# Kernel optimization log

Measured on AMD Instinct MI355X. Metric: run time of the kernel, lower is better.

Reference implementation:

```python
import jax, jax.numpy as jnp
import numpy as np

B, C_IN, H, W = 8, 1024, 18, 80
FEAT = 1024
A = 32      # anchors per location
NCLS = 3    # classes
NREG = 13
K = 3       # kernel size
K2 = K * K
EPS = 1e-5  # BatchNorm eps


def conv2d(x, w, b):
    y = jax.lax.conv_general_dilated(x, w, (1, 1), ((1, 1), (1, 1)),
                                     dimension_numbers=('NCHW', 'OIHW', 'NCHW'))
    return y + b[None, :, None, None]


def bn_eval(x, g, b):
    # eval-mode BatchNorm2d with running_mean=0, running_var=1
    return x * (g / jnp.sqrt(1.0 + EPS))[None, :, None, None] + b[None, :, None, None]


def anchor_flatten(x, d):
    # [B, A*d, H, W] -> permute(0,2,3,1) -> [B, H*W*A, d]
    Bx, Cx, Hx, Wx = x.shape
    return jnp.transpose(x, (0, 2, 3, 1)).reshape(Bx, Hx * Wx * (Cx // d), d)


def bilinear_gather(x, py, px):
    # x: [B,C,H,W]; py/px: [B,K2,H,W] float coords -> [B,C,K2,H,W], zero outside
    Bx, Cx, Hx, Wx = x.shape
    y0 = jnp.floor(py); x0 = jnp.floor(px)
    wy1 = py - y0; wx1 = px - x0
    wy0 = 1.0 - wy1; wx0 = 1.0 - wx1
    xf = x.reshape(Bx, Cx, Hx * Wx)

    def g(yy, xx):
        valid = ((yy >= 0) & (yy < Hx) & (xx >= 0) & (xx < Wx)).astype(x.dtype)
        yc = jnp.clip(yy, 0, Hx - 1).astype(jnp.int32)
        xc = jnp.clip(xx, 0, Wx - 1).astype(jnp.int32)
        idx = (yc * Wx + xc).reshape(Bx, -1)
        vals = jax.vmap(lambda xi, ii: xi[:, ii])(xf, idx).reshape(Bx, Cx, K2, Hx, Wx)
        return vals * valid[:, None]

    return (g(y0, x0) * (wy0 * wx0)[:, None] + g(y0, x0 + 1) * (wy0 * wx1)[:, None]
            + g(y0 + 1, x0) * (wy1 * wx0)[:, None] + g(y0 + 1, x0 + 1) * (wy1 * wx1)[:, None])


def mdcn(x, off_w, off_b, w, b):
    # ModulatedDeformConvPack (DCNv2): 3x3 conv -> (dy, dx, mask), then modulated deform conv
    out = conv2d(x, off_w, off_b)                        # [B, 3*K2, H, W]
    dy, dx, m = out[:, :K2], out[:, K2:2 * K2], jax.nn.sigmoid(out[:, 2 * K2:])
    ky, kx = jnp.meshgrid(jnp.arange(K, dtype=x.dtype), jnp.arange(K, dtype=x.dtype), indexing='ij')
    base_y = jnp.arange(x.shape[2], dtype=x.dtype)[None, None, :, None] - 1.0 + ky.reshape(1, K2, 1, 1)
    base_x = jnp.arange(x.shape[3], dtype=x.dtype)[None, None, None, :] - 1.0 + kx.reshape(1, K2, 1, 1)
    sampled = bilinear_gather(x, base_y + dy, base_x + dx) * m[:, None]   # [B,C,K2,H,W]
    O = w.shape[0]
    return jnp.einsum('bckhw,ock->bohw', sampled, w.reshape(O, w.shape[1], K2)) + b[None, :, None, None]


def setup_inputs() -> dict:
    key = jax.random.key(0)
    ks = jax.random.split(key, 10)
    s1 = 1.0 / np.sqrt(C_IN * K2)
    s2 = 1.0 / np.sqrt(FEAT * K2)
    rn = lambda k, sh, sc: jax.random.normal(k, sh, jnp.float32) * sc
    return {
        'features': jax.random.normal(ks[0], (B, C_IN, H, W), jnp.float32),
        'cls_w1': rn(ks[1], (FEAT, C_IN, K, K), s1), 'cls_b1': jnp.zeros((FEAT,), jnp.float32),
        'cls_w2': rn(ks[2], (FEAT, FEAT, K, K), s2), 'cls_b2': jnp.zeros((FEAT,), jnp.float32),
        'cls_w3': rn(ks[3], (A * NCLS, FEAT, K, K), s2), 'cls_b3': jnp.zeros((A * NCLS,), jnp.float32),
        'off_w': rn(ks[4], (3 * K2, C_IN, K, K), s1), 'off_b': jnp.zeros((3 * K2,), jnp.float32),
        'dcn_w': rn(ks[5], (FEAT, C_IN, K, K), s1), 'dcn_b': jnp.zeros((FEAT,), jnp.float32),
        'bn1_g': jnp.ones((FEAT,), jnp.float32), 'bn1_b': jnp.zeros((FEAT,), jnp.float32),
        'reg_w2': rn(ks[6], (FEAT, FEAT, K, K), s2), 'reg_b2': jnp.zeros((FEAT,), jnp.float32),
        'bn2_g': jnp.ones((FEAT,), jnp.float32), 'bn2_b': jnp.zeros((FEAT,), jnp.float32),
        'reg_w3': rn(ks[7], (A * NREG, FEAT, K, K), s2), 'reg_b3': jnp.zeros((A * NREG,), jnp.float32),
    }


def reference(features, cls_w1, cls_b1, cls_w2, cls_b2, cls_w3, cls_b3,
              off_w, off_b, dcn_w, dcn_b, bn1_g, bn1_b,
              reg_w2, reg_b2, bn2_g, bn2_b, reg_w3, reg_b3):
    # cls branch (Dropout2d is identity in eval)
    h = jax.nn.relu(conv2d(features, cls_w1, cls_b1))
    h = jax.nn.relu(conv2d(h, cls_w2, cls_b2))
    cls_preds = anchor_flatten(conv2d(h, cls_w3, cls_b3), NCLS)   # [B, H*W*A, NCLS]
    # reg branch: modulated deformable conv -> BN -> ReLU -> conv -> BN -> ReLU -> conv
    r = jax.nn.relu(bn_eval(mdcn(features, off_w, off_b, dcn_w, dcn_b), bn1_g, bn1_b))
    r = jax.nn.relu(bn_eval(conv2d(r, reg_w2, reg_b2), bn2_g, bn2_b))
    reg_preds = anchor_flatten(conv2d(r, reg_w3, reg_b3), NREG)   # [B, H*W*A, NREG]
    return (cls_preds, reg_preds)
```

## Files before the change

### kernel.cpp

```cpp
#include <hip/hip_runtime.h>
#include <math.h>

typedef short short8 __attribute__((ext_vector_type(8)));
typedef float f32x4 __attribute__((ext_vector_type(4)));
typedef unsigned short u16;
typedef unsigned int u32;

#define GAS(p) ((__attribute__((address_space(1))) void*)(p))
#define LAS(p) ((__attribute__((address_space(3))) void*)(p))

namespace {

constexpr int HW   = 1440;
constexpr int PBAT = 20 * 82 * 1024;

__device__ __forceinline__ u16 f2bf(float f) {
  u32 u = __float_as_uint(f);
  return (u16)((u + 0x7FFFu + ((u >> 16) & 1u)) >> 16);
}
__device__ __forceinline__ float bf2f(u16 h) {
  return __uint_as_float(((u32)h) << 16);
}

__global__ __launch_bounds__(256)
void transpose_feat(const float* __restrict__ src, u16* __restrict__ dst) {
  __shared__ float tile[128][17];
  const int bh = blockIdx.y;
  const int b = bh / 18, h = bh % 18;
  const int wt = blockIdx.x % 5, ct = blockIdx.x / 5;
  const int w0 = wt * 16, c0 = ct * 128;
  const int tid = threadIdx.x;
#pragma unroll
  for (int it = 0; it < 8; ++it) {
    int idx = it * 256 + tid;
    int c = idx >> 4, w = idx & 15;
    tile[c][w] = src[((size_t)(b * 1024 + c0 + c) * 18 + h) * 80 + w0 + w];
  }
  __syncthreads();
  const int px = tid >> 4, cq = tid & 15;
  union { uint4 u; u16 s[8]; } pk;
#pragma unroll
  for (int j = 0; j < 8; ++j) pk.s[j] = f2bf(tile[cq * 8 + j][px]);
  *(uint4*)(dst + ((size_t)(b * 20 + h + 1) * 82 + (w0 + px + 1)) * 1024 + c0 + cq * 8) = pk.u;
}

struct RepackArgs {
  const float* src[7];
  u16* dst[7];
  int O[7];
  int start[7];
  int nseg;
};

__global__ __launch_bounds__(256)
void repack_all(RepackArgs ra) {
  int blk = blockIdx.x;
  int seg = 0;
#pragma unroll
  for (int i = 1; i < 7; ++i)
    if (i < ra.nseg && blk >= ra.start[i]) seg = i;
  const float* src = ra.src[seg];
  u16* dst = ra.dst[seg];
  const int O = ra.O[seg];
  int idx = (blk - ra.start[seg]) * 256 + threadIdx.x;
  if (idx >= O * 128) return;
  int o = idx >> 7, c8 = idx & 127;
  const float* s = src + (size_t)o * 9216 + (size_t)c8 * 72;
  float v[72];
#pragma unroll
  for (int i = 0; i < 18; ++i) {
    float4 f = *(const float4*)(s + i * 4);
    v[i * 4 + 0] = f.x; v[i * 4 + 1] = f.y; v[i * 4 + 2] = f.z; v[i * 4 + 3] = f.w;
  }
#pragma unroll
  for (int t = 0; t < 9; ++t) {
    union { uint4 u; u16 h[8]; } pk;
#pragma unroll
    for (int j = 0; j < 8; ++j) pk.h[j] = f2bf(v[j * 9 + t]);
    *(uint4*)(dst + ((size_t)t * O + o) * 1024 + c8 * 8) = pk.u;
  }
}

__device__ __forceinline__
void sample_body(int k, int lp, int pix0, int Npc,
                 const u16* __restrict__ featP, const float* __restrict__ offp,
                 u16* __restrict__ spl, int tid) {
  const int p = pix0 + lp;
  const int c8 = tid & 15;
  int b = p / HW, hw = p - b * HW;
  int h = hw / 80, w = hw - h * 80;
  float dy = offp[p * 27 + k];
  float dx = offp[p * 27 + 9 + k];
  float ml = offp[p * 27 + 18 + k];
  float m = 1.f / (1.f + expf(-ml));
  float py = (float)(h - 1 + k / 3) + dy;
  float px = (float)(w - 1 + (k % 3)) + dx;
  float y0f = floorf(py), x0f = floorf(px);
  float wy1 = py - y0f, wx1 = px - x0f;
  float wy0 = 1.f - wy1, wx0 = 1.f - wx1;
  int y0 = (int)y0f, x0 = (int)x0f;
  int ya = min(max(y0, -1), 18),  yb = min(max(y0 + 1, -1), 18);
  int xa = min(max(x0, -1), 80),  xb = min(max(x0 + 1, -1), 80);
  const u16* base = featP + (size_t)b * PBAT;
  const u16* r00 = base + ((size_t)(ya + 1) * 82 + (xa + 1)) * 1024;
  const u16* r01 = base + ((size_t)(ya + 1) * 82 + (xb + 1)) * 1024;
  const u16* r10 = base + ((size_t)(yb + 1) * 82 + (xa + 1)) * 1024;
  const u16* r11 = base + ((size_t)(yb + 1) * 82 + (xb + 1)) * 1024;
  float w00 = wy0 * wx0 * m, w01 = wy0 * wx1 * m;
  float w10 = wy1 * wx0 * m, w11 = wy1 * wx1 * m;
  u16* dst = spl + ((size_t)k * Npc + lp) * 1024;
  for (int c = c8 * 8; c < 1024; c += 128) {
    union { uint4 u; u16 h[8]; } a, bq, cq2, d, o;
    a.u   = *(const uint4*)(r00 + c);
    bq.u  = *(const uint4*)(r01 + c);
    cq2.u = *(const uint4*)(r10 + c);
    d.u   = *(const uint4*)(r11 + c);
#pragma unroll
    for (int j = 0; j < 8; ++j) {
      float v = w00 * bf2f(a.h[j]) + w01 * bf2f(bq.h[j]) +
                w10 * bf2f(cq2.h[j]) + w11 * bf2f(d.h[j]);
      o.h[j] = f2bf(v);
    }
    *(uint4*)(dst + c) = o.u;
  }
}

__global__ __launch_bounds__(256)
void sample_standalone(const u16* __restrict__ featP, const float* __restrict__ offp,
                       u16* __restrict__ spl, int pix0, int Npc) {
  sample_body(blockIdx.y, blockIdx.x * 16 + (threadIdx.x >> 4), pix0, Npc,
              featP, offp, spl, threadIdx.x);
}

struct Job {
  const u16* W; const u16* B;
  const float* bias; const float* bng; const float* bnb;
  void* out; int Co; int pix0; int Npc;
};

template<int FLAGS>
__device__ __forceinline__ void gemm_body(const Job J, int px, int oy) {
  constexpr bool PLANES  = (FLAGS & 1) != 0;
  constexpr bool F32OUT  = (FLAGS & 2) != 0;
  constexpr bool HASBN   = (FLAGS & 4) != 0;
  constexpr bool HASRELU = (FLAGS & 8) != 0;

  __shared__ __align__(16) u16 As[128 * 32];
  __shared__ __align__(16) u16 Bs[128 * 32];
  const int tid = threadIdx.x;
  const int wv = tid >> 6, lane = tid & 63;
  const int o0 = oy * 128;
  const int p0 = J.pix0 + px * 128;

  const int lr = lane >> 2;
  const int qs = (lane & 3) ^ ((lane >> 3) & 3);
  int aoff[2], boff[2];
#pragma unroll
  for (int s = 0; s < 2; ++s) {
    int r = (wv * 2 + s) * 16 + lr;
    int o = min(o0 + r, J.Co - 1);
    aoff[s] = o * 1024 + qs * 8;
    int p = p0 + r;
    if (PLANES) {
      boff[s] = (p - J.pix0) * 1024 + qs * 8;
    } else {
      int b = p / HW, hw = p - b * HW;
      int h = hw / 80, w = hw - h * 80;
      boff[s] = ((b * 20 + h) * 82 + w) * 1024 + qs * 8;
    }
  }
  u16* aDst = As + (wv * 2) * 512;
  u16* bDst = Bs + (wv * 2) * 512;

  const int wm = wv >> 1, wn = wv & 1;
  const int frm = lane & 15;
  const int kq = lane >> 4;
  const int sel = (kq ^ ((lane >> 1) & 3)) * 16;

  f32x4 acc[4][4];
#pragma unroll
  for (int i = 0; i < 4; ++i)
#pragma unroll
    for (int j = 0; j < 4; ++j) acc[i][j] = (f32x4)0.f;

  for (int t = 0; t < 9; ++t) {
    const u16* Wt = J.W + (size_t)t * J.Co * 1024;
    const u16* Bt = J.B + (PLANES ? (size_t)t * (size_t)J.Npc * 1024
                                  : (size_t)(((t / 3) * 82 + (t % 3)) * 1024));
    for (int cc = 0; cc < 1024; cc += 32) {
      __syncthreads();
#pragma unroll
      for (int s = 0; s < 2; ++s) {
        __builtin_amdgcn_global_load_lds(GAS(Wt + aoff[s] + cc), LAS(aDst + s * 512), 16, 0, 0);
        __builtin_amdgcn_global_load_lds(GAS(Bt + boff[s] + cc), LAS(bDst + s * 512), 16, 0, 0);
      }
      __syncthreads();
      uint4 af[4], bf4[4];
#pragma unroll
      for (int i = 0; i < 4; ++i) {
        af[i]  = *(const uint4*)((const char*)As + (wm * 64 + i * 16 + frm) * 64 + sel);
        bf4[i] = *(const uint4*)((const char*)Bs + (wn * 64 + i * 16 + frm) * 64 + sel);
      }
#pragma unroll
      for (int i = 0; i < 4; ++i) {
        short8 a = __builtin_bit_cast(short8, af[i]);
#pragma unroll
        for (int j = 0; j < 4; ++j) {
          short8 b = __builtin_bit_cast(short8, bf4[j]);
          acc[i][j] = __builtin_amdgcn_mfma_f32_16x16x32_bf16(a, b, acc[i][j], 0, 0, 0);
        }
      }
    }
  }

  size_t obase[4];
#pragma unroll
  for (int j = 0; j < 4; ++j) {
    int pn = p0 + wn * 64 + j * 16 + frm;
    if (F32OUT) {
      obase[j] = (size_t)pn * J.Co;
    } else {
      int b = pn / HW, hw = pn - b * HW;
      int h = hw / 80, w = hw - h * 80;
      obase[j] = ((size_t)(b * 20 + h + 1) * 82 + (w + 1)) * 1024;
    }
  }
#pragma unroll
  for (int i = 0; i < 4; ++i) {
    int o = o0 + wm * 64 + i * 16 + kq * 4;
    float bi[4], sc[4], sh[4];
#pragma unroll
    for (int r = 0; r < 4; ++r) {
      int oc = min(o + r, J.Co - 1);
      bi[r] = J.bias[oc];
      if (HASBN) { sc[r] = J.bng[oc] * rsqrtf(1.f + 1e-5f); sh[r] = J.bnb[oc]; }
    }
#pragma unroll
    for (int j = 0; j < 4; ++j) {
      float v[4];
#pragma unroll
      for (int r = 0; r < 4; ++r) {
        float x = acc[i][j][r] + bi[r];
        if (HASBN) x = x * sc[r] + sh[r];
        if (HASRELU) x = fmaxf(x, 0.f);
        v[r] = x;
      }
      if (F32OUT) {
        float* op = (float*)J.out;
#pragma unroll
        for (int r = 0; r < 4; ++r)
          if (o + r < J.Co) op[obase[j] + o + r] = v[r];
      } else {
        u16* op = (u16*)J.out;
        ushort4 pk;
        pk.x = f2bf(v[0]); pk.y = f2bf(v[1]); pk.z = f2bf(v[2]); pk.w = f2bf(v[3]);
        *(ushort4*)(op + obase[j] + o) = pk;
      }
    }
  }
}

template<int F0, int F1>
__global__ __launch_bounds__(256)
void gemm_dual(Job j0, Job j1, int ysplit) {
  int y = blockIdx.y;
  if (y < ysplit) gemm_body<F0>(j0, blockIdx.x, y);
  else            gemm_body<F1>(j1, blockIdx.x, y - ysplit);
}

template<int F0>
__global__ __launch_bounds__(256)
void gemm_sample(Job j, const u16* __restrict__ featP, const float* __restrict__ offp,
                 u16* __restrict__ spl, int gemmBlocks) {
  int gx = blockIdx.x;
  if (gx < gemmBlocks) {
    gemm_body<F0>(j, gx % 90, gx / 90);
  } else {
    int sidx = gx - gemmBlocks;
    int k = sidx / 720, bs = sidx % 720;
    sample_body(k, bs * 16 + (threadIdx.x >> 4), 0, 11520, featP, offp, spl, threadIdx.x);
  }
}

}

extern "C" void kernel_launch(void* const* d_in, const int* in_sizes, int n_in,
                              void* d_out, int out_size, void* d_ws, size_t ws_size,
                              hipStream_t stream) {
  const float* feat   = (const float*)d_in[0];
  const float* cls_w1 = (const float*)d_in[1];
  const float* cls_b1 = (const float*)d_in[2];
  const float* cls_w2 = (const float*)d_in[3];
  const float* cls_b2 = (const float*)d_in[4];
  const float* cls_w3 = (const float*)d_in[5];
  const float* cls_b3 = (const float*)d_in[6];
  const float* off_w  = (const float*)d_in[7];
  const float* off_b  = (const float*)d_in[8];
  const float* dcn_w  = (const float*)d_in[9];
  const float* dcn_b  = (const float*)d_in[10];
  const float* bn1_g  = (const float*)d_in[11];
  const float* bn1_b  = (const float*)d_in[12];
  const float* reg_w2 = (const float*)d_in[13];
  const float* reg_b2 = (const float*)d_in[14];
  const float* bn2_g  = (const float*)d_in[15];
  const float* bn2_b  = (const float*)d_in[16];
  const float* reg_w3 = (const float*)d_in[17];
  const float* reg_b3 = (const float*)d_in[18];
  float* outp = (float*)d_out;

  const size_t ACTB = 26869760;
  char* wsb = (char*)d_ws;
  u16* featP = (u16*)(wsb);
  u16* bufA  = (u16*)(wsb + ACTB);
  u16* bufB  = (u16*)(wsb + 2 * ACTB);
  u16* wts   = (u16*)(wsb + 3 * ACTB);
  float* offp = (float*)(wsb + 3 * ACTB + 85432320);
  u16* spl   = (u16*)(wsb + 3 * ACTB + 85432320 + 1244160);
  const size_t BASE = 3 * ACTB + 85432320 + 1244160;
  const size_t SPLB = (size_t)9 * 11520 * 1024 * 2;

  u16* offT = wts;
  u16* w1T  = wts + 248832;
  u16* w2T  = wts + 9686016;
  u16* w3T  = wts + 19123200;
  u16* dcnT = wts + 20007936;
  u16* r2T  = wts + 29445120;
  u16* r3T  = wts + 38882304;

  dim3 blk(256);

  hipMemsetAsync(featP, 0, 3 * ACTB, stream);
  transpose_feat<<<dim3(40, 144), blk, 0, stream>>>(feat, featP);

  {
    RepackArgs ra;
    const float* s[7] = {off_w, cls_w1, cls_w2, cls_w3, dcn_w, reg_w2, reg_w3};
    u16* d[7] = {offT, w1T, w2T, w3T, dcnT, r2T, r3T};
    int  O[7] = {27, 1024, 1024, 96, 1024, 1024, 416};
    int acc = 0;
    for (int i = 0; i < 7; ++i) {
      ra.src[i] = s[i]; ra.dst[i] = d[i]; ra.O[i] = O[i]; ra.start[i] = acc;
      acc += (O[i] * 128 + 255) / 256;
    }
    ra.nseg = 7;
    repack_all<<<dim3(acc), blk, 0, stream>>>(ra);
  }

  Job jOff  = {offT, featP, off_b, nullptr, nullptr, offp, 27, 0, 0};
  Job jCls1 = {w1T, featP, cls_b1, nullptr, nullptr, bufA, 1024, 0, 0};
  Job jCls2 = {w2T, bufA, cls_b2, nullptr, nullptr, bufB, 1024, 0, 0};
  Job jCls3 = {w3T, bufB, cls_b3, nullptr, nullptr, outp, 96, 0, 0};
  Job jReg2 = {r2T, bufA, reg_b2, bn2_g, bn2_b, bufB, 1024, 0, 0};
  Job jReg3 = {r3T, bufB, reg_b3, nullptr, nullptr, outp + 1105920, 416, 0, 0};

  gemm_dual<8, 2><<<dim3(90, 9), blk, 0, stream>>>(jCls1, jOff, 8);

  if (ws_size >= BASE + SPLB) {
    gemm_sample<8><<<dim3(720 + 6480), blk, 0, stream>>>(jCls2, featP, offp, spl, 720);
    Job jDcn = {dcnT, spl, dcn_b, bn1_g, bn1_b, bufA, 1024, 0, 11520};
    gemm_dual<1 | 4 | 8, 2><<<dim3(90, 9), blk, 0, stream>>>(jDcn, jCls3, 8);
  } else {
    gemm_dual<8, 8><<<dim3(90, 8), blk, 0, stream>>>(jCls2, jCls2, 8);
    size_t avail = ws_size > BASE ? ws_size - BASE : 0;
    int tiles = (int)(avail / 2359296);
    if (tiles < 1) tiles = 1;
    if (tiles > 90) tiles = 90;
    for (int t0 = 0; t0 < 90; t0 += tiles) {
      int nt = (90 - t0) < tiles ? (90 - t0) : tiles;
      int pix0 = t0 * 128, np = nt * 128;
      sample_standalone<<<dim3(nt * 8, 9), blk, 0, stream>>>(featP, offp, spl, pix0, np);
      Job jDcn = {dcnT, spl, dcn_b, bn1_g, bn1_b, bufA, 1024, pix0, np};
      gemm_dual<1 | 4 | 8, 1 | 4 | 8><<<dim3(nt, 8), blk, 0, stream>>>(jDcn, jDcn, 8);
    }
    gemm_dual<2, 2><<<dim3(90, 1), blk, 0, stream>>>(jCls3, jCls3, 1);
  }

  gemm_dual<4 | 8, 4 | 8><<<dim3(90, 8), blk, 0, stream>>>(jReg2, jReg2, 8);
  gemm_dual<2, 2><<<dim3(90, 4), blk, 0, stream>>>(jReg3, jReg3, 4);
}
```

Measured before the change: 2.157 ms.

## Add 256x256-tile 8-wave GEMM with LDS double buffering for large convs

Adds a new GEMM kernel that uses 512 threads and 256x256 output tiles. It double-buffers through a 128KB LDS with direct global-to-LDS loads and interleaves MFMA phases with staging under raised wave priority. The kernel replaces the 128-tile GEMMs for the cls1/offset, cls2+sampling, DCN and reg2 stages, and the co-scheduled sampling blocks are resized to 512 threads. The aim is more data reuse per loaded tile and better overlap of memory and math. The cost is fewer blocks (180–225), which may underfill the GPU's CUs, plus heavier LDS and register use.

```diff
diff --git a/kernel.cpp b/kernel.cpp
--- a/kernel.cpp
+++ b/kernel.cpp
@@ -268,17 +268,200 @@
   else            gemm_body<F1>(j1, blockIdx.x, y - ysplit);
 }
 
+template<int FLAGS>
+__device__ __forceinline__ void gemm8_body(const Job J, char* ldsb, int px, int oy) {
+  constexpr bool PLANES  = (FLAGS & 1) != 0;
+  constexpr bool F32OUT  = (FLAGS & 2) != 0;
+  constexpr bool HASBN   = (FLAGS & 4) != 0;
+  constexpr bool HASRELU = (FLAGS & 8) != 0;
+
+  const int tid = threadIdx.x;
+  const int w = tid >> 6, lane = tid & 63;
+  const int o0 = oy * 256;
+  const int p0 = J.pix0 + px * 256;
+
+  const int lr3 = lane >> 3;
+  const int srcC = ((lane & 7) ^ lr3) << 3;
+  u32 aEl[2][2], bEl[2][2];
+#pragma unroll
+  for (int h = 0; h < 2; ++h)
+#pragma unroll
+  for (int s = 0; s < 2; ++s) {
+    int crow = (w * 2 + s) * 8 + lr3;
+    int o = min(o0 + h * 128 + crow, J.Co - 1);
+    aEl[h][s] = (u32)o * 1024u;
+    int p = p0 + h * 128 + crow;
+    if (PLANES) {
+      bEl[h][s] = (u32)(p - J.pix0) * 1024u;
+    } else {
+      int b = p / HW, hw = p - b * HW;
+      int hh = hw / 80, ww = hw - hh * 80;
+      bEl[h][s] = (u32)((b * 20 + hh) * 82 + ww) * 1024u;
+    }
+  }
+
+  auto STAGE_A = [&](int buf, int h, int kt) {
+    int tap = kt >> 4, cc = (kt & 15) << 6;
+    const u16* src = J.W + (size_t)tap * (size_t)J.Co * 1024 + cc + srcC;
+    char* dst = ldsb + (buf * 65536 + h * 16384 + (w * 2) * 1024);
+    __builtin_amdgcn_global_load_lds(GAS(src + aEl[h][0]), LAS(dst), 16, 0, 0);
+    __builtin_amdgcn_global_load_lds(GAS(src + aEl[h][1]), LAS(dst + 1024), 16, 0, 0);
+  };
+  auto STAGE_B = [&](int buf, int h, int kt) {
+    int tap = kt >> 4, cc = (kt & 15) << 6;
+    size_t tb = PLANES ? (size_t)tap * (size_t)J.Npc * 1024
+                       : (size_t)(((tap / 3) * 82 + (tap % 3)) * 1024);
+    const u16* src = J.B + tb + cc + srcC;
+    char* dst = ldsb + (buf * 65536 + 32768 + h * 16384 + (w * 2) * 1024);
+    __builtin_amdgcn_global_load_lds(GAS(src + bEl[h][0]), LAS(dst), 16, 0, 0);
+    __builtin_amdgcn_global_load_lds(GAS(src + bEl[h][1]), LAS(dst + 1024), 16, 0, 0);
+  };
+
+  const int wm2 = w >> 2, wn2 = w & 3;
+  const int rA = wm2 * 64 + (lane & 15);
+  const int rB = wn2 * 32 + (lane & 15);
+  const int xsw = (lane & 7) << 4;
+  const int csw0 = (((lane >> 4) << 4)) ^ xsw;
+  const int csw1 = (64 | ((lane >> 4) << 4)) ^ xsw;
+
+  f32x4 acc[4][4][2];
+#pragma unroll
+  for (int q = 0; q < 4; ++q)
+#pragma unroll
+  for (int m = 0; m < 4; ++m)
+#pragma unroll
+  for (int n = 0; n < 2; ++n) acc[q][m][n] = (f32x4)0.f;
+
+  uint4 aF[4][2], bF[2][2];
+
+#define G8_RD_A(BUF, AH)                                                      \
+  { const char* Ab_ = ldsb + ((BUF) * 65536 + (AH) * 16384);                  \
+    _Pragma("unroll") for (int m_ = 0; m_ < 4; ++m_) {                        \
+      aF[m_][0] = *(const uint4*)(Ab_ + (rA + m_ * 16) * 128 + csw0);         \
+      aF[m_][1] = *(const uint4*)(Ab_ + (rA + m_ * 16) * 128 + csw1); } }
+
+#define G8_RD_B(BUF, BH)                                                      \
+  { const char* Bb_ = ldsb + ((BUF) * 65536 + 32768 + (BH) * 16384);          \
+    _Pragma("unroll") for (int n_ = 0; n_ < 2; ++n_) {                        \
+      bF[n_][0] = *(const uint4*)(Bb_ + (rB + n_ * 16) * 128 + csw0);         \
+      bF[n_][1] = *(const uint4*)(Bb_ + (rB + n_ * 16) * 128 + csw1); } }
+
+#define G8_MMA(Q)                                                             \
+    __builtin_amdgcn_s_barrier();                                             \
+    asm volatile("s_waitcnt lgkmcnt(0)" ::: "memory");                        \
+    __builtin_amdgcn_sched_barrier(0);                                        \
+    __builtin_amdgcn_s_setprio(1);                                            \
+    _Pragma("unroll") for (int m_ = 0; m_ < 4; ++m_)                          \
+    _Pragma("unroll") for (int n_ = 0; n_ < 2; ++n_)                          \
+    _Pragma("unroll") for (int k_ = 0; k_ < 2; ++k_)                          \
+      acc[Q][m_][n_] = __builtin_amdgcn_mfma_f32_16x16x32_bf16(               \
+          __builtin_bit_cast(short8, aF[m_][k_]),                             \
+          __builtin_bit_cast(short8, bF[n_][k_]), acc[Q][m_][n_], 0, 0, 0);   \
+    __builtin_amdgcn_s_setprio(0);
+
+#define G8_VMW asm volatile("s_waitcnt vmcnt(4)" ::: "memory");
+#define G8_BAR __builtin_amdgcn_s_barrier();
+
+  STAGE_A(0, 0, 0); STAGE_A(0, 1, 0); STAGE_B(0, 0, 0); STAGE_B(0, 1, 0);
+  STAGE_A(1, 0, 1); STAGE_B(1, 0, 1);
+  G8_VMW
+  __builtin_amdgcn_s_barrier();
+
+  for (int it = 0; it < 72; ++it) {
+    const int kt = it * 2;
+    const int k2 = min(kt + 2, 143), k3 = min(kt + 3, 143);
+    G8_RD_A(0, 0) G8_RD_B(0, 0) STAGE_B(1, 1, kt + 1); G8_MMA(0) G8_BAR
+    G8_RD_B(0, 1)               STAGE_A(1, 1, kt + 1); G8_MMA(1) G8_BAR
+    G8_RD_A(0, 1) G8_RD_B(0, 0) STAGE_A(0, 0, k2);     G8_MMA(2) G8_BAR
+    G8_RD_B(0, 1)               STAGE_B(0, 0, k2);     G8_MMA(3) G8_VMW G8_BAR
+    G8_RD_A(1, 0) G8_RD_B(1, 0) STAGE_B(0, 1, k2);     G8_MMA(0) G8_BAR
+    G8_RD_B(1, 1)               STAGE_A(0, 1, k2);     G8_MMA(1) G8_BAR
+    G8_RD_A(1, 1) G8_RD_B(1, 0) STAGE_A(1, 0, k3);     G8_MMA(2) G8_BAR
+    G8_RD_B(1, 1)               STAGE_B(1, 0, k3);     G8_MMA(3) G8_VMW G8_BAR
+  }
+
+#undef G8_RD_A
+#undef G8_RD_B
+#undef G8_MMA
+#undef G8_VMW
+#undef G8_BAR
+
+  const int kq = lane >> 4, fr = lane & 15;
+  size_t pixB[2][2];
+#pragma unroll
+  for (int bh = 0; bh < 2; ++bh)
+#pragma unroll
+  for (int n = 0; n < 2; ++n) {
+    int p = p0 + bh * 128 + wn2 * 32 + n * 16 + fr;
+    if (F32OUT) {
+      pixB[bh][n] = (size_t)p * J.Co;
+    } else {
+      int b = p / HW, hw = p - b * HW;
+      int hh = hw / 80, ww = hw - hh * 80;
+      pixB[bh][n] = ((size_t)(b * 20 + hh + 1) * 82 + (ww + 1)) * 1024;
+    }
+  }
+#pragma unroll
+  for (int ah = 0; ah < 2; ++ah)
+#pragma unroll
+  for (int m = 0; m < 4; ++m) {
+    int ob = o0 + ah * 128 + wm2 * 64 + m * 16 + kq * 4;
+    float bi[4], sc[4], sh[4];
+#pragma unroll
+    for (int r = 0; r < 4; ++r) {
+      int oc = min(ob + r, J.Co - 1);
+      bi[r] = J.bias[oc];
+      if (HASBN) { sc[r] = J.bng[oc] * rsqrtf(1.f + 1e-5f); sh[r] = J.bnb[oc]; }
+    }
+#pragma unroll
+    for (int bh = 0; bh < 2; ++bh)
+#pragma unroll
+    for (int n = 0; n < 2; ++n) {
+      float v[4];
+#pragma unroll
+      for (int r = 0; r < 4; ++r) {
+        float x = acc[ah * 2 + bh][m][n][r] + bi[r];
+        if (HASBN) x = x * sc[r] + sh[r];
+        if (HASRELU) x = fmaxf(x, 0.f);
+        v[r] = x;
+      }
+      if (F32OUT) {
+        float* op = (float*)J.out;
+#pragma unroll
+        for (int r = 0; r < 4; ++r)
+          if (ob + r < J.Co) op[pixB[bh][n] + ob + r] = v[r];
+      } else {
+        u16* op = (u16*)J.out;
+        ushort4 pk;
+        pk.x = f2bf(v[0]); pk.y = f2bf(v[1]); pk.z = f2bf(v[2]); pk.w = f2bf(v[3]);
+        *(ushort4*)(op + pixB[bh][n] + ob) = pk;
+      }
+    }
+  }
+}
+
+template<int F0, int F1>
+__global__ __launch_bounds__(512, 2)
+void gemm8_dual(Job j0, Job j1, int n0, int mt0, int mt1) {
+  __shared__ __align__(16) char ldsb[131072];
+  int x = blockIdx.x;
+  if (x < n0) gemm8_body<F0>(j0, ldsb, x / mt0, x % mt0);
+  else { x -= n0; gemm8_body<F1>(j1, ldsb, x / mt1, x % mt1); }
+}
+
 template<int F0>
-__global__ __launch_bounds__(256)
-void gemm_sample(Job j, const u16* __restrict__ featP, const float* __restrict__ offp,
-                 u16* __restrict__ spl, int gemmBlocks) {
-  int gx = blockIdx.x;
-  if (gx < gemmBlocks) {
-    gemm_body<F0>(j, gx % 90, gx / 90);
+__global__ __launch_bounds__(512, 2)
+void gemm8_sample(Job j, const u16* __restrict__ featP, const float* __restrict__ offp,
+                  u16* __restrict__ spl, int n0, int mt0) {
+  __shared__ __align__(16) char ldsb[131072];
+  int x = blockIdx.x;
+  if (x < n0) {
+    gemm8_body<F0>(j, ldsb, x / mt0, x % mt0);
   } else {
-    int sidx = gx - gemmBlocks;
-    int k = sidx / 720, bs = sidx % 720;
-    sample_body(k, bs * 16 + (threadIdx.x >> 4), 0, 11520, featP, offp, spl, threadIdx.x);
+    int sidx = x - n0;
+    int k = sidx / 360, bs = sidx % 360;
+    sample_body(k, bs * 32 + ((int)threadIdx.x >> 4), 0, 11520,
+                featP, offp, spl, (int)threadIdx.x);
   }
 }
 
@@ -353,13 +536,16 @@
   Job jReg2 = {r2T, bufA, reg_b2, bn2_g, bn2_b, bufB, 1024, 0, 0};
   Job jReg3 = {r3T, bufB, reg_b3, nullptr, nullptr, outp + 1105920, 416, 0, 0};
 
-  gemm_dual<8, 2><<<dim3(90, 9), blk, 0, stream>>>(jCls1, jOff, 8);
-
   if (ws_size >= BASE + SPLB) {
-    gemm_sample<8><<<dim3(720 + 6480), blk, 0, stream>>>(jCls2, featP, offp, spl, 720);
+    dim3 b512(512);
+    gemm8_dual<8, 2><<<dim3(225), b512, 0, stream>>>(jCls1, jOff, 180, 4, 1);
+    gemm8_sample<8><<<dim3(180 + 3240), b512, 0, stream>>>(jCls2, featP, offp, spl, 180, 4);
     Job jDcn = {dcnT, spl, dcn_b, bn1_g, bn1_b, bufA, 1024, 0, 11520};
-    gemm_dual<1 | 4 | 8, 2><<<dim3(90, 9), blk, 0, stream>>>(jDcn, jCls3, 8);
+    gemm8_dual<1 | 4 | 8, 2><<<dim3(225), b512, 0, stream>>>(jDcn, jCls3, 180, 4, 1);
+    gemm8_dual<4 | 8, 4 | 8><<<dim3(180), b512, 0, stream>>>(jReg2, jReg2, 180, 4, 4);
+    gemm_dual<2, 2><<<dim3(90, 4), blk, 0, stream>>>(jReg3, jReg3, 4);
   } else {
+    gemm_dual<8, 2><<<dim3(90, 9), blk, 0, stream>>>(jCls1, jOff, 8);
     gemm_dual<8, 8><<<dim3(90, 8), blk, 0, stream>>>(jCls2, jCls2, 8);
     size_t avail = ws_size > BASE ? ws_size - BASE : 0;
     int tiles = (int)(avail / 2359296);
@@ -373,8 +559,7 @@
       gemm_dual<1 | 4 | 8, 1 | 4 | 8><<<dim3(nt, 8), blk, 0, stream>>>(jDcn, jDcn, 8);
     }
     gemm_dual<2, 2><<<dim3(90, 1), blk, 0, stream>>>(jCls3, jCls3, 1);
-  }
-
-  gemm_dual<4 | 8, 4 | 8><<<dim3(90, 8), blk, 0, stream>>>(jReg2, jReg2, 8);
-  gemm_dual<2, 2><<<dim3(90, 4), blk, 0, stream>>>(jReg3, jReg3, 4);
-}
+    gemm_dual<4 | 8, 4 | 8><<<dim3(90, 8), blk, 0, stream>>>(jReg2, jReg2, 8);
+    gemm_dual<2, 2><<<dim3(90, 4), blk, 0, stream>>>(jReg3, jReg3, 4);
+  }
+}
```

Result: no change. 2.161 ms (+0.2%).

## Triple-buffer GEMM LDS staging and pipeline chunked DCN sampling with GEMM

Applied to the files above, without the earlier changes.

The GEMM inner loop moves from a single LDS buffer with two barriers per K-step to a three-stage ring. Global-to-LDS loads for step k+2 are issued before the MFMAs for step k, with vmcnt waits, so load latency is hidden. A new mid-workspace path splits the deformable sampling into chunks and double-buffers them: each launch runs the DCN GEMM on the current chunk and samples the next chunk concurrently. Triple buffering raises LDS per block to 48KB, which may reduce occupancy.

```diff
diff --git a/kernel.cpp b/kernel.cpp
--- a/kernel.cpp
+++ b/kernel.cpp
@@ -145,8 +145,8 @@
   constexpr bool HASBN   = (FLAGS & 4) != 0;
   constexpr bool HASRELU = (FLAGS & 8) != 0;
 
-  __shared__ __align__(16) u16 As[128 * 32];
-  __shared__ __align__(16) u16 Bs[128 * 32];
+  __shared__ __align__(16) u16 As[3 * 4096];
+  __shared__ __align__(16) u16 Bs[3 * 4096];
   const int tid = threadIdx.x;
   const int wv = tid >> 6, lane = tid & 63;
   const int o0 = oy * 128;
@@ -169,8 +169,6 @@
       boff[s] = ((b * 20 + h) * 82 + w) * 1024 + qs * 8;
     }
   }
-  u16* aDst = As + (wv * 2) * 512;
-  u16* bDst = Bs + (wv * 2) * 512;
 
   const int wm = wv >> 1, wn = wv & 1;
   const int frm = lane & 15;
@@ -183,35 +181,57 @@
 #pragma unroll
     for (int j = 0; j < 4; ++j) acc[i][j] = (f32x4)0.f;
 
-  for (int t = 0; t < 9; ++t) {
-    const u16* Wt = J.W + (size_t)t * J.Co * 1024;
-    const u16* Bt = J.B + (PLANES ? (size_t)t * (size_t)J.Npc * 1024
-                                  : (size_t)(((t / 3) * 82 + (t % 3)) * 1024));
-    for (int cc = 0; cc < 1024; cc += 32) {
-      __syncthreads();
-#pragma unroll
-      for (int s = 0; s < 2; ++s) {
-        __builtin_amdgcn_global_load_lds(GAS(Wt + aoff[s] + cc), LAS(aDst + s * 512), 16, 0, 0);
-        __builtin_amdgcn_global_load_lds(GAS(Bt + boff[s] + cc), LAS(bDst + s * 512), 16, 0, 0);
-      }
-      __syncthreads();
-      uint4 af[4], bf4[4];
-#pragma unroll
-      for (int i = 0; i < 4; ++i) {
-        af[i]  = *(const uint4*)((const char*)As + (wm * 64 + i * 16 + frm) * 64 + sel);
-        bf4[i] = *(const uint4*)((const char*)Bs + (wn * 64 + i * 16 + frm) * 64 + sel);
-      }
-#pragma unroll
-      for (int i = 0; i < 4; ++i) {
-        short8 a = __builtin_bit_cast(short8, af[i]);
-#pragma unroll
-        for (int j = 0; j < 4; ++j) {
-          short8 b = __builtin_bit_cast(short8, bf4[j]);
-          acc[i][j] = __builtin_amdgcn_mfma_f32_16x16x32_bf16(a, b, acc[i][j], 0, 0, 0);
-        }
-      }
-    }
-  }
+#define GB_STAGE(ST, KK)                                                      \
+  { int t_ = (KK) >> 5, c0_ = ((KK) & 31) << 5;                               \
+    const u16* Wt_ = J.W + (size_t)t_ * (size_t)J.Co * 1024 + c0_;            \
+    const u16* Bt_ = J.B + (PLANES ? (size_t)t_ * (size_t)J.Npc * 1024        \
+                     : (size_t)(((t_ / 3) * 82 + (t_ % 3)) * 1024)) + c0_;    \
+    u16* aD_ = As + (ST) * 4096 + (wv * 2) * 512;                             \
+    u16* bD_ = Bs + (ST) * 4096 + (wv * 2) * 512;                             \
+    __builtin_amdgcn_global_load_lds(GAS(Wt_ + aoff[0]), LAS(aD_),       16, 0, 0); \
+    __builtin_amdgcn_global_load_lds(GAS(Wt_ + aoff[1]), LAS(aD_ + 512), 16, 0, 0); \
+    __builtin_amdgcn_global_load_lds(GAS(Bt_ + boff[0]), LAS(bD_),       16, 0, 0); \
+    __builtin_amdgcn_global_load_lds(GAS(Bt_ + boff[1]), LAS(bD_ + 512), 16, 0, 0); }
+
+#define GB_MMA(ST)                                                            \
+  { const char* Ab_ = (const char*)As + (ST) * 8192;                          \
+    const char* Bb_ = (const char*)Bs + (ST) * 8192;                          \
+    uint4 af[4], bf4[4];                                                      \
+    _Pragma("unroll") for (int i_ = 0; i_ < 4; ++i_) {                        \
+      af[i_]  = *(const uint4*)(Ab_ + (wm * 64 + i_ * 16 + frm) * 64 + sel);  \
+      bf4[i_] = *(const uint4*)(Bb_ + (wn * 64 + i_ * 16 + frm) * 64 + sel); }\
+    _Pragma("unroll") for (int i_ = 0; i_ < 4; ++i_) {                        \
+      short8 a_ = __builtin_bit_cast(short8, af[i_]);                         \
+      _Pragma("unroll") for (int j_ = 0; j_ < 4; ++j_) {                      \
+        short8 b_ = __builtin_bit_cast(short8, bf4[j_]);                      \
+        acc[i_][j_] = __builtin_amdgcn_mfma_f32_16x16x32_bf16(a_, b_, acc[i_][j_], 0, 0, 0); } } }
+
+#define GB_STEP(ST, NB, KS, DOST, VMN)                                        \
+  { if (DOST) GB_STAGE(NB, KS)                                                \
+    GB_MMA(ST)                                                                \
+    asm volatile("s_waitcnt vmcnt(" #VMN ")" ::: "memory");                   \
+    __builtin_amdgcn_s_barrier();                                             \
+    asm volatile("" ::: "memory"); }
+
+  GB_STAGE(0, 0)
+  GB_STAGE(1, 1)
+  asm volatile("s_waitcnt vmcnt(4)" ::: "memory");
+  __builtin_amdgcn_s_barrier();
+  asm volatile("" ::: "memory");
+
+  for (int i = 0; i < 95; ++i) {
+    const int kk = i * 3;
+    GB_STEP(0, 2, kk + 2, true, 4)
+    GB_STEP(1, 0, kk + 3, true, 4)
+    GB_STEP(2, 1, kk + 4, true, 4)
+  }
+  GB_STEP(0, 2, 287, true, 4)
+  GB_STEP(1, 0, 0, false, 0)
+  GB_MMA(2)
+
+#undef GB_STAGE
+#undef GB_MMA
+#undef GB_STEP
 
   size_t obase[4];
 #pragma unroll
@@ -271,15 +291,33 @@
 template<int F0>
 __global__ __launch_bounds__(256)
 void gemm_sample(Job j, const u16* __restrict__ featP, const float* __restrict__ offp,
-                 u16* __restrict__ spl, int gemmBlocks) {
+                 u16* __restrict__ spl, int n0, int pix0s, int nps) {
   int gx = blockIdx.x;
-  if (gx < gemmBlocks) {
+  if (gx < n0) {
     gemm_body<F0>(j, gx % 90, gx / 90);
   } else {
-    int sidx = gx - gemmBlocks;
-    int k = sidx / 720, bs = sidx % 720;
-    sample_body(k, bs * 16 + (threadIdx.x >> 4), 0, 11520, featP, offp, spl, threadIdx.x);
-  }
+    int sidx = gx - n0;
+    int per = nps >> 4;
+    int k = sidx / per, bs = sidx % per;
+    sample_body(k, bs * 16 + ((int)threadIdx.x >> 4), pix0s, nps,
+                featP, offp, spl, (int)threadIdx.x);
+  }
+}
+
+template<int F0, int F1>
+__global__ __launch_bounds__(256)
+void dcn_chunk(Job j0, Job j1, int n0, int nt0, int n1,
+               const u16* __restrict__ featP, const float* __restrict__ offp,
+               u16* __restrict__ splNext, int pix0n, int npn) {
+  int x = blockIdx.x;
+  if (x < n0) { gemm_body<F0>(j0, x % nt0, x / nt0); return; }
+  x -= n0;
+  if (x < n1) { gemm_body<F1>(j1, x % 90, x / 90); return; }
+  x -= n1;
+  int per = npn >> 4;
+  int k = x / per, bs = x % per;
+  sample_body(k, bs * 16 + ((int)threadIdx.x >> 4), pix0n, npn,
+              featP, offp, splNext, (int)threadIdx.x);
 }
 
 }
@@ -353,28 +391,59 @@
   Job jReg2 = {r2T, bufA, reg_b2, bn2_g, bn2_b, bufB, 1024, 0, 0};
   Job jReg3 = {r3T, bufB, reg_b3, nullptr, nullptr, outp + 1105920, 416, 0, 0};
 
+  size_t avail = ws_size > BASE ? ws_size - BASE : 0;
+
+  int tch = 0;
+  {
+    const int cand[5] = {30, 18, 15, 10, 9};
+    for (int i = 0; i < 5; ++i)
+      if ((size_t)2 * cand[i] * 2359296 <= avail) { tch = cand[i]; break; }
+  }
+
   gemm_dual<8, 2><<<dim3(90, 9), blk, 0, stream>>>(jCls1, jOff, 8);
 
-  if (ws_size >= BASE + SPLB) {
-    gemm_sample<8><<<dim3(720 + 6480), blk, 0, stream>>>(jCls2, featP, offp, spl, 720);
+  if (avail >= SPLB) {
+    gemm_sample<8><<<dim3(720 + 6480), blk, 0, stream>>>(jCls2, featP, offp, spl, 720, 0, 11520);
     Job jDcn = {dcnT, spl, dcn_b, bn1_g, bn1_b, bufA, 1024, 0, 11520};
     gemm_dual<1 | 4 | 8, 2><<<dim3(90, 9), blk, 0, stream>>>(jDcn, jCls3, 8);
+    gemm_dual<4 | 8, 4 | 8><<<dim3(90, 8), blk, 0, stream>>>(jReg2, jReg2, 8);
+    gemm_dual<2, 2><<<dim3(90, 4), blk, 0, stream>>>(jReg3, jReg3, 4);
+  } else if (tch > 0) {
+    const int C = 90 / tch;
+    const int np = tch * 128;
+    u16* splA = spl;
+    u16* splB = spl + (size_t)tch * 1179648;
+
+    gemm_sample<8><<<dim3(720 + 9 * (np / 16)), blk, 0, stream>>>(
+        jCls2, featP, offp, splA, 720, 0, np);
+    for (int i = 0; i < C; ++i) {
+      u16* sCur  = (i & 1) ? splB : splA;
+      u16* sNext = (i & 1) ? splA : splB;
+      Job jDcnC = {dcnT, sCur, dcn_b, bn1_g, bn1_b, bufA, 1024, i * np, np};
+      int n0 = tch * 8;
+      int n1 = (i == 0) ? 90 : 0;
+      bool hasS = (i + 1 < C);
+      int ns = hasS ? 9 * (np / 16) : 0;
+      dcn_chunk<1 | 4 | 8, 2><<<dim3(n0 + n1 + ns), blk, 0, stream>>>(
+          jDcnC, jCls3, n0, tch, n1,
+          featP, offp, sNext, (i + 1) * np, hasS ? np : 16);
+    }
+    gemm_dual<4 | 8, 4 | 8><<<dim3(90, 8), blk, 0, stream>>>(jReg2, jReg2, 8);
+    gemm_dual<2, 2><<<dim3(90, 4), blk, 0, stream>>>(jReg3, jReg3, 4);
   } else {
     gemm_dual<8, 8><<<dim3(90, 8), blk, 0, stream>>>(jCls2, jCls2, 8);
-    size_t avail = ws_size > BASE ? ws_size - BASE : 0;
     int tiles = (int)(avail / 2359296);
     if (tiles < 1) tiles = 1;
     if (tiles > 90) tiles = 90;
     for (int t0 = 0; t0 < 90; t0 += tiles) {
       int nt = (90 - t0) < tiles ? (90 - t0) : tiles;
-      int pix0 = t0 * 128, np = nt * 128;
-      sample_standalone<<<dim3(nt * 8, 9), blk, 0, stream>>>(featP, offp, spl, pix0, np);
-      Job jDcn = {dcnT, spl, dcn_b, bn1_g, bn1_b, bufA, 1024, pix0, np};
+      int pix0 = t0 * 128, npp = nt * 128;
+      sample_standalone<<<dim3(nt * 8, 9), blk, 0, stream>>>(featP, offp, spl, pix0, npp);
+      Job jDcn = {dcnT, spl, dcn_b, bn1_g, bn1_b, bufA, 1024, pix0, npp};
       gemm_dual<1 | 4 | 8, 1 | 4 | 8><<<dim3(nt, 8), blk, 0, stream>>>(jDcn, jDcn, 8);
     }
     gemm_dual<2, 2><<<dim3(90, 1), blk, 0, stream>>>(jCls3, jCls3, 1);
-  }
-
-  gemm_dual<4 | 8, 4 | 8><<<dim3(90, 8), blk, 0, stream>>>(jReg2, jReg2, 8);
-  gemm_dual<2, 2><<<dim3(90, 4), blk, 0, stream>>>(jReg3, jReg3, 4);
-}
+    gemm_dual<4 | 8, 4 | 8><<<dim3(90, 8), blk, 0, stream>>>(jReg2, jReg2, 8);
+    gemm_dual<2, 2><<<dim3(90, 4), blk, 0, stream>>>(jReg3, jReg3, 4);
+  }
+}
```

Result: slower. 2.984 ms (+38.3%).

## Fuse deformable bilinear sampling into DCN GEMM B-tile load, deepen K step

Applied to the files above, without the earlier changes.

Replaces the separate sampling pass, which wrote a 9-plane bf16 sampled tensor to global memory, with a small prep kernel. The prep kernel precomputes four corner offsets and four modulated weights per pixel and tap. The DCN GEMM then gathers and blends the four corners directly into LDS while loading its B tile, which removes the large intermediate write and read. The GEMM also now loads 64 channels per barrier pair instead of 32, and block IDs are remapped so neighbouring tiles land on the same XCD. In exchange, the DCN GEMM does the gather and blend work on every one of its 8 output-row tiles, repeating it up to 8x, and it no longer overlaps sampling with the cls2 GEMM.

```diff
diff --git a/kernel.cpp b/kernel.cpp
--- a/kernel.cpp
+++ b/kernel.cpp
@@ -20,6 +20,12 @@
 }
 __device__ __forceinline__ float bf2f(u16 h) {
   return __uint_as_float(((u32)h) << 16);
+}
+
+__device__ __forceinline__ int xcd_virt(int id, int N) {
+  int q = N >> 3, r = N & 7;
+  int xcd = id & 7, pos = id >> 3;
+  return (xcd < r ? xcd * (q + 1) : r * (q + 1) + (xcd - r) * q) + pos;
 }
 
 __global__ __launch_bounds__(256)
@@ -81,12 +87,11 @@
   }
 }
 
-__device__ __forceinline__
-void sample_body(int k, int lp, int pix0, int Npc,
-                 const u16* __restrict__ featP, const float* __restrict__ offp,
-                 u16* __restrict__ spl, int tid) {
-  const int p = pix0 + lp;
-  const int c8 = tid & 15;
+__global__ __launch_bounds__(256)
+void prep_off(const float* __restrict__ offp, u32* __restrict__ prep) {
+  int idx = blockIdx.x * 256 + threadIdx.x;
+  if (idx >= 9 * 11520) return;
+  int k = idx / 11520, p = idx - k * 11520;
   int b = p / HW, hw = p - b * HW;
   int h = hw / 80, w = hw - h * 80;
   float dy = offp[p * 27 + k];
@@ -101,122 +106,71 @@
   int y0 = (int)y0f, x0 = (int)x0f;
   int ya = min(max(y0, -1), 18),  yb = min(max(y0 + 1, -1), 18);
   int xa = min(max(x0, -1), 80),  xb = min(max(x0 + 1, -1), 80);
-  const u16* base = featP + (size_t)b * PBAT;
-  const u16* r00 = base + ((size_t)(ya + 1) * 82 + (xa + 1)) * 1024;
-  const u16* r01 = base + ((size_t)(ya + 1) * 82 + (xb + 1)) * 1024;
-  const u16* r10 = base + ((size_t)(yb + 1) * 82 + (xa + 1)) * 1024;
-  const u16* r11 = base + ((size_t)(yb + 1) * 82 + (xb + 1)) * 1024;
-  float w00 = wy0 * wx0 * m, w01 = wy0 * wx1 * m;
-  float w10 = wy1 * wx0 * m, w11 = wy1 * wx1 * m;
-  u16* dst = spl + ((size_t)k * Npc + lp) * 1024;
-  for (int c = c8 * 8; c < 1024; c += 128) {
-    union { uint4 u; u16 h[8]; } a, bq, cq2, d, o;
-    a.u   = *(const uint4*)(r00 + c);
-    bq.u  = *(const uint4*)(r01 + c);
-    cq2.u = *(const uint4*)(r10 + c);
-    d.u   = *(const uint4*)(r11 + c);
-#pragma unroll
-    for (int j = 0; j < 8; ++j) {
-      float v = w00 * bf2f(a.h[j]) + w01 * bf2f(bq.h[j]) +
-                w10 * bf2f(cq2.h[j]) + w11 * bf2f(d.h[j]);
-      o.h[j] = f2bf(v);
-    }
-    *(uint4*)(dst + c) = o.u;
-  }
-}
-
-__global__ __launch_bounds__(256)
-void sample_standalone(const u16* __restrict__ featP, const float* __restrict__ offp,
-                       u16* __restrict__ spl, int pix0, int Npc) {
-  sample_body(blockIdx.y, blockIdx.x * 16 + (threadIdx.x >> 4), pix0, Npc,
-              featP, offp, spl, threadIdx.x);
+  u32 base = (u32)b * PBAT;
+  uint4 ov;
+  ov.x = base + ((u32)(ya + 1) * 82 + (u32)(xa + 1)) * 1024;
+  ov.y = base + ((u32)(ya + 1) * 82 + (u32)(xb + 1)) * 1024;
+  ov.z = base + ((u32)(yb + 1) * 82 + (u32)(xa + 1)) * 1024;
+  ov.w = base + ((u32)(yb + 1) * 82 + (u32)(xb + 1)) * 1024;
+  float4 wv4;
+  wv4.x = wy0 * wx0 * m; wv4.y = wy0 * wx1 * m;
+  wv4.z = wy1 * wx0 * m; wv4.w = wy1 * wx1 * m;
+  u32* dst = prep + (size_t)idx * 8;
+  *(uint4*)dst = ov;
+  *(float4*)(dst + 4) = wv4;
 }
 
 struct Job {
   const u16* W; const u16* B;
   const float* bias; const float* bng; const float* bnb;
   void* out; int Co; int pix0; int Npc;
+  const u32* prep;
 };
 
+constexpr int LDSU16 = 16384;
+
+struct GemmAddr {
+  int aoff[2], boff[2];
+  int wm, wn, frm, kq, sel, wv;
+};
+
+__device__ __forceinline__ GemmAddr gemm_addr(const Job& J, int px, int oy) {
+  GemmAddr G;
+  const int tid = threadIdx.x;
+  G.wv = tid >> 6;
+  const int lane = tid & 63;
+  const int o0 = oy * 128;
+  const int p0 = J.pix0 + px * 128;
+  const int lr = lane >> 2;
+  const int qs = (lane & 3) ^ ((lane >> 3) & 3);
+#pragma unroll
+  for (int s = 0; s < 2; ++s) {
+    int r = (G.wv * 2 + s) * 16 + lr;
+    int o = min(o0 + r, J.Co - 1);
+    G.aoff[s] = o * 1024 + qs * 8;
+    int p = p0 + r;
+    int b = p / HW, hw = p - b * HW;
+    int h = hw / 80, w = hw - h * 80;
+    G.boff[s] = ((b * 20 + h) * 82 + w) * 1024 + qs * 8;
+  }
+  G.wm = G.wv >> 1; G.wn = G.wv & 1;
+  G.frm = lane & 15; G.kq = lane >> 4;
+  G.sel = (G.kq ^ ((lane >> 1) & 3)) * 16;
+  return G;
+}
+
 template<int FLAGS>
-__device__ __forceinline__ void gemm_body(const Job J, int px, int oy) {
-  constexpr bool PLANES  = (FLAGS & 1) != 0;
+__device__ __forceinline__ void gemm_epilogue(const Job& J, const GemmAddr& G,
+                                              f32x4 (&acc)[4][4], int px, int oy) {
   constexpr bool F32OUT  = (FLAGS & 2) != 0;
   constexpr bool HASBN   = (FLAGS & 4) != 0;
   constexpr bool HASRELU = (FLAGS & 8) != 0;
-
-  __shared__ __align__(16) u16 As[128 * 32];
-  __shared__ __align__(16) u16 Bs[128 * 32];
-  const int tid = threadIdx.x;
-  const int wv = tid >> 6, lane = tid & 63;
   const int o0 = oy * 128;
   const int p0 = J.pix0 + px * 128;
-
-  const int lr = lane >> 2;
-  const int qs = (lane & 3) ^ ((lane >> 3) & 3);
-  int aoff[2], boff[2];
-#pragma unroll
-  for (int s = 0; s < 2; ++s) {
-    int r = (wv * 2 + s) * 16 + lr;
-    int o = min(o0 + r, J.Co - 1);
-    aoff[s] = o * 1024 + qs * 8;
-    int p = p0 + r;
-    if (PLANES) {
-      boff[s] = (p - J.pix0) * 1024 + qs * 8;
-    } else {
-      int b = p / HW, hw = p - b * HW;
-      int h = hw / 80, w = hw - h * 80;
-      boff[s] = ((b * 20 + h) * 82 + w) * 1024 + qs * 8;
-    }
-  }
-  u16* aDst = As + (wv * 2) * 512;
-  u16* bDst = Bs + (wv * 2) * 512;
-
-  const int wm = wv >> 1, wn = wv & 1;
-  const int frm = lane & 15;
-  const int kq = lane >> 4;
-  const int sel = (kq ^ ((lane >> 1) & 3)) * 16;
-
-  f32x4 acc[4][4];
-#pragma unroll
-  for (int i = 0; i < 4; ++i)
-#pragma unroll
-    for (int j = 0; j < 4; ++j) acc[i][j] = (f32x4)0.f;
-
-  for (int t = 0; t < 9; ++t) {
-    const u16* Wt = J.W + (size_t)t * J.Co * 1024;
-    const u16* Bt = J.B + (PLANES ? (size_t)t * (size_t)J.Npc * 1024
-                                  : (size_t)(((t / 3) * 82 + (t % 3)) * 1024));
-    for (int cc = 0; cc < 1024; cc += 32) {
-      __syncthreads();
-#pragma unroll
-      for (int s = 0; s < 2; ++s) {
-        __builtin_amdgcn_global_load_lds(GAS(Wt + aoff[s] + cc), LAS(aDst + s * 512), 16, 0, 0);
-        __builtin_amdgcn_global_load_lds(GAS(Bt + boff[s] + cc), LAS(bDst + s * 512), 16, 0, 0);
-      }
-      __syncthreads();
-      uint4 af[4], bf4[4];
-#pragma unroll
-      for (int i = 0; i < 4; ++i) {
-        af[i]  = *(const uint4*)((const char*)As + (wm * 64 + i * 16 + frm) * 64 + sel);
-        bf4[i] = *(const uint4*)((const char*)Bs + (wn * 64 + i * 16 + frm) * 64 + sel);
-      }
-#pragma unroll
-      for (int i = 0; i < 4; ++i) {
-        short8 a = __builtin_bit_cast(short8, af[i]);
-#pragma unroll
-        for (int j = 0; j < 4; ++j) {
-          short8 b = __builtin_bit_cast(short8, bf4[j]);
-          acc[i][j] = __builtin_amdgcn_mfma_f32_16x16x32_bf16(a, b, acc[i][j], 0, 0, 0);
-        }
-      }
-    }
-  }
-
   size_t obase[4];
 #pragma unroll
   for (int j = 0; j < 4; ++j) {
-    int pn = p0 + wn * 64 + j * 16 + frm;
+    int pn = p0 + G.wn * 64 + j * 16 + G.frm;
     if (F32OUT) {
       obase[j] = (size_t)pn * J.Co;
     } else {
@@ -227,7 +181,7 @@
   }
 #pragma unroll
   for (int i = 0; i < 4; ++i) {
-    int o = o0 + wm * 64 + i * 16 + kq * 4;
+    int o = o0 + G.wm * 64 + i * 16 + G.kq * 4;
     float bi[4], sc[4], sh[4];
 #pragma unroll
     for (int r = 0; r < 4; ++r) {
@@ -260,26 +214,109 @@
   }
 }
 
+template<int FLAGS>
+__device__ __forceinline__ void gemm_body(const Job J, u16* lds, int px, int oy) {
+  constexpr bool FUSED = (FLAGS & 16) != 0;
+  u16* As = lds;
+  u16* Bs = lds + 8192;
+  GemmAddr G = gemm_addr(J, px, oy);
+  u16* aDst = As + (G.wv * 2) * 512;
+  u16* bDst = Bs + (G.wv * 2) * 512;
+
+  const int tid = threadIdx.x;
+  const int lane = tid & 63;
+  const int lr = lane >> 2;
+  const int qs8 = ((lane & 3) ^ ((lane >> 3) & 3)) * 8;
+  const int p0 = J.pix0 + px * 128;
+
+  f32x4 acc[4][4];
+#pragma unroll
+  for (int i = 0; i < 4; ++i)
+#pragma unroll
+    for (int j = 0; j < 4; ++j) acc[i][j] = (f32x4)0.f;
+
+  for (int t = 0; t < 9; ++t) {
+    const u16* Wt = J.W + (size_t)t * J.Co * 1024;
+    const u16* Bt = J.B + (size_t)(((t / 3) * 82 + (t % 3)) * 1024);
+    uint4 po[2]; float4 pw[2];
+    if (FUSED) {
+#pragma unroll
+      for (int s = 0; s < 2; ++s) {
+        int p = p0 + (G.wv * 2 + s) * 16 + lr;
+        const u32* pr = J.prep + ((size_t)t * 11520 + p) * 8;
+        po[s] = *(const uint4*)pr;
+        pw[s] = *(const float4*)(pr + 4);
+      }
+    }
+    for (int cc = 0; cc < 1024; cc += 64) {
+      __syncthreads();
+#pragma unroll
+      for (int s2 = 0; s2 < 2; ++s2)
+#pragma unroll
+        for (int s = 0; s < 2; ++s) {
+          __builtin_amdgcn_global_load_lds(GAS(Wt + G.aoff[s] + cc + s2 * 32),
+                                           LAS(aDst + s2 * 4096 + s * 512), 16, 0, 0);
+          if (!FUSED)
+            __builtin_amdgcn_global_load_lds(GAS(Bt + G.boff[s] + cc + s2 * 32),
+                                             LAS(bDst + s2 * 4096 + s * 512), 16, 0, 0);
+        }
+      if (FUSED) {
+        const u16* fp = J.B;
+#pragma unroll
+        for (int s = 0; s < 2; ++s)
+#pragma unroll
+          for (int s2 = 0; s2 < 2; ++s2) {
+            int chb = cc + s2 * 32 + qs8;
+            union { uint4 u; u16 h[8]; } c0, c1, c2, c3, ob;
+            c0.u = *(const uint4*)(fp + po[s].x + chb);
+            c1.u = *(const uint4*)(fp + po[s].y + chb);
+            c2.u = *(const uint4*)(fp + po[s].z + chb);
+            c3.u = *(const uint4*)(fp + po[s].w + chb);
+#pragma unroll
+            for (int j = 0; j < 8; ++j) {
+              float v = pw[s].x * bf2f(c0.h[j]) + pw[s].y * bf2f(c1.h[j]) +
+                        pw[s].z * bf2f(c2.h[j]) + pw[s].w * bf2f(c3.h[j]);
+              ob.h[j] = f2bf(v);
+            }
+            *(uint4*)(Bs + s2 * 4096 + (G.wv * 2 + s) * 512 + lane * 8) = ob.u;
+          }
+      }
+      __syncthreads();
+#pragma unroll
+      for (int s2 = 0; s2 < 2; ++s2) {
+        const char* Ab = (const char*)As + s2 * 8192;
+        const char* Bb = (const char*)Bs + s2 * 8192;
+        uint4 af[4], bf4[4];
+#pragma unroll
+        for (int i = 0; i < 4; ++i) {
+          af[i]  = *(const uint4*)(Ab + (G.wm * 64 + i * 16 + G.frm) * 64 + G.sel);
+          bf4[i] = *(const uint4*)(Bb + (G.wn * 64 + i * 16 + G.frm) * 64 + G.sel);
+        }
+#pragma unroll
+        for (int i = 0; i < 4; ++i) {
+          short8 a = __builtin_bit_cast(short8, af[i]);
+#pragma unroll
+          for (int j = 0; j < 4; ++j) {
+            short8 b = __builtin_bit_cast(short8, bf4[j]);
+            acc[i][j] = __builtin_amdgcn_mfma_f32_16x16x32_bf16(a, b, acc[i][j], 0, 0, 0);
+          }
+        }
+      }
+    }
+  }
+  gemm_epilogue<FLAGS>(J, G, acc, px, oy);
+}
+
 template<int F0, int F1>
 __global__ __launch_bounds__(256)
 void gemm_dual(Job j0, Job j1, int ysplit) {
-  int y = blockIdx.y;
-  if (y < ysplit) gemm_body<F0>(j0, blockIdx.x, y);
-  else            gemm_body<F1>(j1, blockIdx.x, y - ysplit);
-}
-
-template<int F0>
-__global__ __launch_bounds__(256)
-void gemm_sample(Job j, const u16* __restrict__ featP, const float* __restrict__ offp,
-                 u16* __restrict__ spl, int gemmBlocks) {
-  int gx = blockIdx.x;
-  if (gx < gemmBlocks) {
-    gemm_body<F0>(j, gx % 90, gx / 90);
-  } else {
-    int sidx = gx - gemmBlocks;
-    int k = sidx / 720, bs = sidx % 720;
-    sample_body(k, bs * 16 + (threadIdx.x >> 4), 0, 11520, featP, offp, spl, threadIdx.x);
-  }
+  __shared__ __align__(16) u16 lds[LDSU16];
+  int id = blockIdx.y * gridDim.x + blockIdx.x;
+  int virt = xcd_virt(id, gridDim.x * gridDim.y);
+  int NY = gridDim.y;
+  int px = virt / NY, y = virt % NY;
+  if (y < ysplit) gemm_body<F0>(j0, lds, px, y);
+  else            gemm_body<F1>(j1, lds, px, y - ysplit);
 }
 
 }
@@ -315,9 +352,7 @@
   u16* bufB  = (u16*)(wsb + 2 * ACTB);
   u16* wts   = (u16*)(wsb + 3 * ACTB);
   float* offp = (float*)(wsb + 3 * ACTB + 85432320);
-  u16* spl   = (u16*)(wsb + 3 * ACTB + 85432320 + 1244160);
-  const size_t BASE = 3 * ACTB + 85432320 + 1244160;
-  const size_t SPLB = (size_t)9 * 11520 * 1024 * 2;
+  u32* prep  = (u32*)(wsb + 3 * ACTB + 85432320 + 1244160);
 
   u16* offT = wts;
   u16* w1T  = wts + 248832;
@@ -346,35 +381,18 @@
     repack_all<<<dim3(acc), blk, 0, stream>>>(ra);
   }
 
-  Job jOff  = {offT, featP, off_b, nullptr, nullptr, offp, 27, 0, 0};
-  Job jCls1 = {w1T, featP, cls_b1, nullptr, nullptr, bufA, 1024, 0, 0};
-  Job jCls2 = {w2T, bufA, cls_b2, nullptr, nullptr, bufB, 1024, 0, 0};
-  Job jCls3 = {w3T, bufB, cls_b3, nullptr, nullptr, outp, 96, 0, 0};
-  Job jReg2 = {r2T, bufA, reg_b2, bn2_g, bn2_b, bufB, 1024, 0, 0};
-  Job jReg3 = {r3T, bufB, reg_b3, nullptr, nullptr, outp + 1105920, 416, 0, 0};
+  Job jOff  = {offT, featP, off_b, nullptr, nullptr, offp, 27, 0, 0, nullptr};
+  Job jCls1 = {w1T, featP, cls_b1, nullptr, nullptr, bufA, 1024, 0, 0, nullptr};
+  Job jCls2 = {w2T, bufA, cls_b2, nullptr, nullptr, bufB, 1024, 0, 0, nullptr};
+  Job jCls3 = {w3T, bufB, cls_b3, nullptr, nullptr, outp, 96, 0, 0, nullptr};
+  Job jDcn  = {dcnT, featP, dcn_b, bn1_g, bn1_b, bufA, 1024, 0, 0, prep};
+  Job jReg2 = {r2T, bufA, reg_b2, bn2_g, bn2_b, bufB, 1024, 0, 0, nullptr};
+  Job jReg3 = {r3T, bufB, reg_b3, nullptr, nullptr, outp + 1105920, 416, 0, 0, nullptr};
 
   gemm_dual<8, 2><<<dim3(90, 9), blk, 0, stream>>>(jCls1, jOff, 8);
-
-  if (ws_size >= BASE + SPLB) {
-    gemm_sample<8><<<dim3(720 + 6480), blk, 0, stream>>>(jCls2, featP, offp, spl, 720);
-    Job jDcn = {dcnT, spl, dcn_b, bn1_g, bn1_b, bufA, 1024, 0, 11520};
-    gemm_dual<1 | 4 | 8, 2><<<dim3(90, 9), blk, 0, stream>>>(jDcn, jCls3, 8);
-  } else {
-    gemm_dual<8, 8><<<dim3(90, 8), blk, 0, stream>>>(jCls2, jCls2, 8);
-    size_t avail = ws_size > BASE ? ws_size - BASE : 0;
-    int tiles = (int)(avail / 2359296);
-    if (tiles < 1) tiles = 1;
-    if (tiles > 90) tiles = 90;
-    for (int t0 = 0; t0 < 90; t0 += tiles) {
-      int nt = (90 - t0) < tiles ? (90 - t0) : tiles;
-      int pix0 = t0 * 128, np = nt * 128;
-      sample_standalone<<<dim3(nt * 8, 9), blk, 0, stream>>>(featP, offp, spl, pix0, np);
-      Job jDcn = {dcnT, spl, dcn_b, bn1_g, bn1_b, bufA, 1024, pix0, np};
-      gemm_dual<1 | 4 | 8, 1 | 4 | 8><<<dim3(nt, 8), blk, 0, stream>>>(jDcn, jDcn, 8);
-    }
-    gemm_dual<2, 2><<<dim3(90, 1), blk, 0, stream>>>(jCls3, jCls3, 1);
-  }
-
+  prep_off<<<dim3(405), blk, 0, stream>>>(offp, prep);
+  gemm_dual<8, 8><<<dim3(90, 8), blk, 0, stream>>>(jCls2, jCls2, 8);
+  gemm_dual<16 | 4 | 8, 2><<<dim3(90, 9), blk, 0, stream>>>(jDcn, jCls3, 8);
   gemm_dual<4 | 8, 4 | 8><<<dim3(90, 8), blk, 0, stream>>>(jReg2, jReg2, 8);
   gemm_dual<2, 2><<<dim3(90, 4), blk, 0, stream>>>(jReg3, jReg3, 4);
 }
```

Result: faster. 1.841 ms (-14.6%).
